# Performance work log

Hardware: AMD Instinct MI355X
Metric: run time of the kernel (lower is better)

Reference implementation:

```python
import jax, jax.numpy as jnp
import numpy as np
import math

B, N, T, F_IN, F_OUT = 32, 512, 12, 64, 64


def setup_inputs() -> dict:
    key = jax.random.key(0)
    k1, k2, k3 = jax.random.split(key, 3)
    x = jax.random.normal(k1, (B, N, T, F_IN), dtype=jnp.float32)
    adj = jax.random.uniform(k2, (N, N), dtype=jnp.float32)  # sym_norm_Adj_matrix
    W_theta = jax.random.normal(k3, (F_OUT, F_IN), dtype=jnp.float32) * (1.0 / math.sqrt(F_IN))
    return {"x": x, "adj": adj, "W_theta": W_theta}


def reference(x, adj, W_theta):
    # x: (B, N, T, F)
    b, n, t, f = x.shape
    scale = 1.0 / math.sqrt(f)
    # (B, T, N, F)
    xt = jnp.transpose(x, (0, 2, 1, 3))
    # attention scores per (batch, time): QK^T / sqrt(F), softmax over last dim,
    # then an extra 1/sqrt(F) scaling as in the original forward
    score = jnp.einsum('btnf,btmf->btnm', xt, xt) * scale
    att = jax.nn.softmax(score, axis=-1) * scale  # dropout p=0
    # post-softmax multiplicative adjacency mask, then aggregate neighbor features
    agg = jnp.einsum('btnm,btmf->btnf', adj[None, None] * att, xt)
    # Theta linear (no bias) + ReLU, back to (B, N, T, F_out)
    out = jax.nn.relu(jnp.einsum('btnf,of->btno', agg, W_theta))
    return jnp.transpose(out, (0, 2, 1, 3))
```

## Files before the change

### kernel.cpp

```cpp
#include <hip/hip_runtime.h>
#include <math.h>

#define NN 512
#define TT 12
#define FF 64

typedef float  f32x4   __attribute__((ext_vector_type(4)));
typedef float  f32x16  __attribute__((ext_vector_type(16)));
typedef short  short4v __attribute__((ext_vector_type(4)));
typedef short  short8v __attribute__((ext_vector_type(8)));
typedef _Float16 h16x4 __attribute__((ext_vector_type(4)));
typedef _Float16 h16x8 __attribute__((ext_vector_type(8)));
typedef unsigned int u32;
typedef u32    u32x4   __attribute__((ext_vector_type(4)));

static __device__ __forceinline__ u32 pkrtz(float a, float b) {
    u32 p;
    asm("v_cvt_pkrtz_f16_f32 %0, %1, %2" : "=v"(p) : "v"(a), "v"(b));
    return p;
}
static __device__ __forceinline__ void cvt4h(f32x4 v, short4v& h, short4v& lo) {
    h16x4 hh, ll;
    #pragma unroll
    for (int j = 0; j < 4; ++j) {
        _Float16 a = (_Float16)v[j];
        hh[j] = a;
        ll[j] = (_Float16)(v[j] - (float)a);
    }
    h  = __builtin_bit_cast(short4v, hh);
    lo = __builtin_bit_cast(short4v, ll);
}
static __device__ __forceinline__ short4v cvt4hi(f32x4 v) {
    h16x4 hh;
    #pragma unroll
    for (int j = 0; j < 4; ++j) hh[j] = (_Float16)v[j];
    return __builtin_bit_cast(short4v, hh);
}
static __device__ __forceinline__ short8v cat44(short4v a, short4v b) {
    return __builtin_shufflevector(a, b, 0, 1, 2, 3, 4, 5, 6, 7);
}
static __device__ __forceinline__ f32x16 mfmah(short8v a, short8v b, f32x16 c) {
    return __builtin_amdgcn_mfma_f32_32x32x16_f16(
        __builtin_bit_cast(h16x8, a), __builtin_bit_cast(h16x8, b), c, 0, 0, 0);
}

#define BUFSZ 17408
#define SMEM_BYTES 52736

__global__ __launch_bounds__(256, 3)
void sgcn19(const float* __restrict__ x, const float* __restrict__ adj,
            const float* __restrict__ W, float* __restrict__ out)
{
    __shared__ __align__(16) char smem[SMEM_BYTES];
    char* sA = smem;
    float* linvLDS = (float*)(smem + 3 * BUFSZ);

    const int d   = blockIdx.x;
    const int xcd = d & 7;
    const int s   = d >> 3;
    const int G   = xcd + 8 * (s >> 2);
    const int mem = s & 3;
    const int t = G % TT, b = G / TT;
    const int n0 = mem * 128;

    const int tid = threadIdx.x;
    const int w   = tid >> 6;
    const int l31 = tid & 31;
    const int hi2 = (tid >> 5) & 1;
    const int fq  = tid & 15;
    const int mq  = tid >> 4;
    const int myn = n0 + 32 * w + l31;

    const float K2 = 0.18033688011112042f;
    const float SH2 = 8.656170245333781f;

    const float* xnrow = x + ((size_t)(b * NN + myn) * TT + t) * FF;
    short8v xnH[4];
    #pragma unroll
    for (int ks = 0; ks < 4; ++ks) {
        f32x4 a0 = *(const f32x4*)(xnrow + ks * 16 + hi2 * 8);
        f32x4 a1 = *(const f32x4*)(xnrow + ks * 16 + hi2 * 8 + 4);
        xnH[ks] = cat44(cvt4hi(a0), cvt4hi(a1));
    }

    short4v sh[4];

#define STAGE_LOAD(M0, R0, R1, R2, R3)                                         \
    {                                                                          \
        const float* xs = x + ((size_t)(b * NN + (M0) + 4 * mq) * TT + t) * FF + 4 * fq; \
        R0 = *(const f32x4*)(xs);                                              \
        R1 = *(const f32x4*)(xs + TT * FF);                                    \
        R2 = *(const f32x4*)(xs + 2 * TT * FF);                                \
        R3 = *(const f32x4*)(xs + 3 * TT * FF);                                \
    }

#define STAGE_CONVERT(L0, L1, L2, L3)                                          \
    { sh[0] = cvt4hi(L0); sh[1] = cvt4hi(L1);                                  \
      sh[2] = cvt4hi(L2); sh[3] = cvt4hi(L3); }

#define STAGE_LDS_WRITE(DST)                                                   \
  {                                                                            \
    char* dKH = (DST);                                                         \
    char* dKT = (DST) + 8704;                                                  \
    _Pragma("unroll")                                                          \
    for (int j = 0; j < 4; ++j)                                                \
        *(short4v*)(dKH + ((4*mq+j)*68 + 4*fq) * 2) = sh[j];                   \
    _Pragma("unroll")                                                          \
    for (int j = 0; j < 4; ++j) {                                              \
        short4v th; th[0]=sh[0][j]; th[1]=sh[1][j]; th[2]=sh[2][j]; th[3]=sh[3][j]; \
        *(short4v*)(dKT + ((4*fq+j)*68 + 4*mq) * 2) = th;                      \
    }                                                                          \
  }

#define PROCESS_TILE(BASE, M0)                                                 \
  {                                                                            \
    const char* bKH = (BASE);                                                  \
    const char* bKT = (BASE) + 8704;                                           \
    const float* arow0 = adj + (size_t)myn * NN + (M0) + 4 * hi2;              \
    f32x4 a00 = *(const f32x4*)(arow0);                                        \
    f32x4 a01 = *(const f32x4*)(arow0 + 8);                                    \
    f32x4 a02 = *(const f32x4*)(arow0 + 16);                                   \
    f32x4 a03 = *(const f32x4*)(arow0 + 24);                                   \
    short8v pa[4];                                                             \
    f32x16 sc;                                                                 \
    _Pragma("unroll")                                                          \
    for (int i = 0; i < 16; ++i) sc[i] = 0.f;                                  \
    _Pragma("unroll")                                                          \
    for (int ks = 0; ks < 4; ++ks) {                                           \
        short4v k0 = *(const short4v*)(bKH + (l31 * 68 + ks*16 + hi2*8) * 2);  \
        short4v k1 = *(const short4v*)(bKH + (l31 * 68 + ks*16 + hi2*8 + 4) * 2); \
        sc = mfmah(cat44(k0, k1), xnH[ks], sc);                                \
    }                                                                          \
    const float* arow1 = adj + (size_t)myn * NN + (M0) + 32 + 4 * hi2;         \
    f32x4 a10 = *(const f32x4*)(arow1);                                        \
    f32x4 a11 = *(const f32x4*)(arow1 + 8);                                    \
    f32x4 a12 = *(const f32x4*)(arow1 + 16);                                   \
    f32x4 a13 = *(const f32x4*)(arow1 + 24);                                   \
    {                                                                          \
        float p[16];                                                           \
        _Pragma("unroll")                                                      \
        for (int r = 0; r < 16; ++r) {                                         \
            p[r] = __builtin_amdgcn_exp2f(sc[r] * K2 - SH2);                   \
            lp4[r & 3] += p[r];                                                \
        }                                                                      \
        p[0] *= a00[0]; p[1] *= a00[1]; p[2]  *= a00[2]; p[3]  *= a00[3];      \
        p[4] *= a01[0]; p[5] *= a01[1]; p[6]  *= a01[2]; p[7]  *= a01[3];      \
        p[8] *= a02[0]; p[9] *= a02[1]; p[10] *= a02[2]; p[11] *= a02[3];      \
        p[12]*= a03[0]; p[13]*= a03[1]; p[14] *= a03[2]; p[15] *= a03[3];      \
        u32x4 e, o;                                                            \
        e[0] = pkrtz(p[0],  p[1]);  e[1] = pkrtz(p[2],  p[3]);                 \
        e[2] = pkrtz(p[4],  p[5]);  e[3] = pkrtz(p[6],  p[7]);                 \
        o[0] = pkrtz(p[8],  p[9]);  o[1] = pkrtz(p[10], p[11]);                \
        o[2] = pkrtz(p[12], p[13]); o[3] = pkrtz(p[14], p[15]);                \
        pa[0] = __builtin_bit_cast(short8v, e);                                \
        pa[1] = __builtin_bit_cast(short8v, o);                                \
    }                                                                          \
    {                                                                          \
        short4v v0 = *(const short4v*)(bKT + (l31 * 68 + 4*hi2) * 2);          \
        short4v v1 = *(const short4v*)(bKT + (l31 * 68 + 8 + 4*hi2) * 2);      \
        agg0 = mfmah(pa[0], cat44(v0, v1), agg0);                              \
        short4v w0 = *(const short4v*)(bKT + ((32 + l31) * 68 + 4*hi2) * 2);   \
        short4v w1 = *(const short4v*)(bKT + ((32 + l31) * 68 + 8 + 4*hi2) * 2); \
        agg1 = mfmah(pa[0], cat44(w0, w1), agg1);                              \
        short4v v2 = *(const short4v*)(bKT + (l31 * 68 + 16 + 4*hi2) * 2);     \
        short4v v3 = *(const short4v*)(bKT + (l31 * 68 + 16 + 8 + 4*hi2) * 2); \
        agg0 = mfmah(pa[1], cat44(v2, v3), agg0);                              \
        short4v w2 = *(const short4v*)(bKT + ((32 + l31) * 68 + 16 + 4*hi2) * 2); \
        short4v w3 = *(const short4v*)(bKT + ((32 + l31) * 68 + 16 + 8 + 4*hi2) * 2); \
        agg1 = mfmah(pa[1], cat44(w2, w3), agg1);                              \
    }                                                                          \
    _Pragma("unroll")                                                          \
    for (int i = 0; i < 16; ++i) sc[i] = 0.f;                                  \
    _Pragma("unroll")                                                          \
    for (int ks = 0; ks < 4; ++ks) {                                           \
        short4v k0 = *(const short4v*)(bKH + ((32 + l31) * 68 + ks*16 + hi2*8) * 2); \
        short4v k1 = *(const short4v*)(bKH + ((32 + l31) * 68 + ks*16 + hi2*8 + 4) * 2); \
        sc = mfmah(cat44(k0, k1), xnH[ks], sc);                                \
    }                                                                          \
    {                                                                          \
        float p[16];                                                           \
        _Pragma("unroll")                                                      \
        for (int r = 0; r < 16; ++r) {                                         \
            p[r] = __builtin_amdgcn_exp2f(sc[r] * K2 - SH2);                   \
            lp4[r & 3] += p[r];                                                \
        }                                                                      \
        p[0] *= a10[0]; p[1] *= a10[1]; p[2]  *= a10[2]; p[3]  *= a10[3];      \
        p[4] *= a11[0]; p[5] *= a11[1]; p[6]  *= a11[2]; p[7]  *= a11[3];      \
        p[8] *= a12[0]; p[9] *= a12[1]; p[10] *= a12[2]; p[11] *= a12[3];      \
        p[12]*= a13[0]; p[13]*= a13[1]; p[14] *= a13[2]; p[15] *= a13[3];      \
        u32x4 e, o;                                                            \
        e[0] = pkrtz(p[0],  p[1]);  e[1] = pkrtz(p[2],  p[3]);                 \
        e[2] = pkrtz(p[4],  p[5]);  e[3] = pkrtz(p[6],  p[7]);                 \
        o[0] = pkrtz(p[8],  p[9]);  o[1] = pkrtz(p[10], p[11]);                \
        o[2] = pkrtz(p[12], p[13]); o[3] = pkrtz(p[14], p[15]);                \
        pa[2] = __builtin_bit_cast(short8v, e);                                \
        pa[3] = __builtin_bit_cast(short8v, o);                                \
    }                                                                          \
    {                                                                          \
        short4v v0 = *(const short4v*)(bKT + (l31 * 68 + 32 + 4*hi2) * 2);     \
        short4v v1 = *(const short4v*)(bKT + (l31 * 68 + 32 + 8 + 4*hi2) * 2); \
        agg0 = mfmah(pa[2], cat44(v0, v1), agg0);                              \
        short4v w0 = *(const short4v*)(bKT + ((32 + l31) * 68 + 32 + 4*hi2) * 2); \
        short4v w1 = *(const short4v*)(bKT + ((32 + l31) * 68 + 32 + 8 + 4*hi2) * 2); \
        agg1 = mfmah(pa[2], cat44(w0, w1), agg1);                              \
        short4v v2 = *(const short4v*)(bKT + (l31 * 68 + 48 + 4*hi2) * 2);     \
        short4v v3 = *(const short4v*)(bKT + (l31 * 68 + 48 + 8 + 4*hi2) * 2); \
        agg0 = mfmah(pa[3], cat44(v2, v3), agg0);                              \
        short4v w2 = *(const short4v*)(bKT + ((32 + l31) * 68 + 48 + 4*hi2) * 2); \
        short4v w3 = *(const short4v*)(bKT + ((32 + l31) * 68 + 48 + 8 + 4*hi2) * 2); \
        agg1 = mfmah(pa[3], cat44(w2, w3), agg1);                              \
    }                                                                          \
  }

    {
        f32x4 l0, l1, l2, l3;
        STAGE_LOAD(0, l0, l1, l2, l3)
        STAGE_CONVERT(l0, l1, l2, l3)
        STAGE_LDS_WRITE(smem)
        STAGE_LOAD(64, l0, l1, l2, l3)
        STAGE_CONVERT(l0, l1, l2, l3)
        STAGE_LDS_WRITE(smem + BUFSZ)
    }
    __syncthreads();

    float lp4[4] = {0.f, 0.f, 0.f, 0.f};
    f32x16 agg0, agg1;
    #pragma unroll
    for (int i = 0; i < 16; ++i) { agg0[i] = 0.f; agg1[i] = 0.f; }

    unsigned A = 0, B = BUFSZ, C = 2 * BUFSZ;
    for (int win = 0; win < 4; ++win) {
        const int ta = 2 * win;

        f32x4 q0, q1, q2, q3;
        if (win < 3) STAGE_LOAD((ta + 2) * 64, q0, q1, q2, q3)

        PROCESS_TILE(smem + A, ta * 64)

        f32x4 r0, r1, r2, r3;
        if (win < 3) {
            STAGE_CONVERT(q0, q1, q2, q3)
            STAGE_LDS_WRITE(smem + C)
            STAGE_LOAD((ta + 3) * 64, r0, r1, r2, r3)
        }

        PROCESS_TILE(smem + B, ta * 64 + 64)

        if (win < 3) STAGE_CONVERT(r0, r1, r2, r3)
        __syncthreads();
        if (win < 3) STAGE_LDS_WRITE(smem + A)
        __syncthreads();

        unsigned tmp = A; A = C; C = B; B = tmp;
    }

    float lpart = (lp4[0] + lp4[1]) + (lp4[2] + lp4[3]);
    float lf = lpart + __shfl_xor(lpart, 32);
    if (hi2 == 0) linvLDS[32 * w + l31] = 0.125f / lf;
    __syncthreads();

    #pragma unroll
    for (int r = 0; r < 16; ++r) {
        int row = 32 * w + (r & 3) + 8 * (r >> 2) + 4 * hi2;
        float nv = linvLDS[row];
        _Float16 h0 = (_Float16)(agg0[r] * nv);
        _Float16 h1 = (_Float16)(agg1[r] * nv);
        *(short*)(sA + (row * 68 + l31) * 2)      = __builtin_bit_cast(short, h0);
        *(short*)(sA + (row * 68 + 32 + l31) * 2) = __builtin_bit_cast(short, h1);
    }
    __syncthreads();

    short8v gH[4];
    #pragma unroll
    for (int ks = 0; ks < 4; ++ks) {
        short4v a0 = *(const short4v*)(sA + ((32*w + l31) * 68 + ks*16 + hi2*8) * 2);
        short4v a1 = *(const short4v*)(sA + ((32*w + l31) * 68 + ks*16 + hi2*8 + 4) * 2);
        gH[ks] = cat44(a0, a1);
    }

    #pragma unroll
    for (int ob = 0; ob < 2; ++ob) {
        short8v wHreg[4], wLreg[4];
        #pragma unroll
        for (int ks = 0; ks < 4; ++ks) {
            const float* wp = W + (size_t)(ob * 32 + l31) * FF + ks * 16 + hi2 * 8;
            f32x4 wa = *(const f32x4*)(wp);
            f32x4 wb = *(const f32x4*)(wp + 4);
            short4v h0, l0, h1, l1;
            cvt4h(wa, h0, l0);
            cvt4h(wb, h1, l1);
            wHreg[ks] = cat44(h0, h1);
            wLreg[ks] = cat44(l0, l1);
        }
        f32x16 oc;
        #pragma unroll
        for (int i = 0; i < 16; ++i) oc[i] = 0.f;
        #pragma unroll
        for (int ks = 0; ks < 4; ++ks) {
            oc = mfmah(gH[ks], wHreg[ks], oc);
            oc = mfmah(gH[ks], wLreg[ks], oc);
        }
        #pragma unroll
        for (int r = 0; r < 16; ++r) {
            int row = 32 * w + (r & 3) + 8 * (r >> 2) + 4 * hi2;
            out[((size_t)(b * NN + n0 + row) * TT + t) * FF + 32 * ob + l31] = fmaxf(oc[r], 0.f);
        }
    }
#undef STAGE_LOAD
#undef STAGE_CONVERT
#undef STAGE_LDS_WRITE
#undef PROCESS_TILE
}

extern "C" void kernel_launch(void* const* d_in, const int* in_sizes, int n_in,
                              void* d_out, int out_size, void* d_ws, size_t ws_size,
                              hipStream_t stream) {
    const float* x   = (const float*)d_in[0];
    const float* adj = (const float*)d_in[1];
    const float* W   = (const float*)d_in[2];
    float* outp = (float*)d_out;

    sgcn19<<<dim3(1536), dim3(256), 0, stream>>>(x, adj, W, outp);
}
```

Before: 77.44 us.

## Use 512-thread blocks covering 256 rows with double-buffered K tiles

Each block now has 512 threads (8 waves) and handles 256 query rows per (b,t) instead of 128, so every staged 64-row K/V tile in LDS is shared by twice as many rows and the grid is halved. The triple-buffered two-tiles-per-iteration pipeline becomes a simpler double buffer with one tile per iteration and a single barrier per tile. Each thread now loads two rows per stage instead of four, and the transposed LDS writes shrink to 2-element stores. This cuts redundant global loads of x and LDS traffic, at the cost of more threads per barrier, a shallower prefetch pipeline and possibly different occupancy.

```diff
diff --git a/kernel.cpp b/kernel.cpp
--- a/kernel.cpp
+++ b/kernel.cpp
@@ -7,6 +7,7 @@
 
 typedef float  f32x4   __attribute__((ext_vector_type(4)));
 typedef float  f32x16  __attribute__((ext_vector_type(16)));
+typedef short  short2v __attribute__((ext_vector_type(2)));
 typedef short  short4v __attribute__((ext_vector_type(4)));
 typedef short  short8v __attribute__((ext_vector_type(8)));
 typedef _Float16 h16x4 __attribute__((ext_vector_type(4)));
@@ -45,23 +46,23 @@
 }
 
 #define BUFSZ 17408
-#define SMEM_BYTES 52736
-
-__global__ __launch_bounds__(256, 3)
-void sgcn19(const float* __restrict__ x, const float* __restrict__ adj,
+#define SMEM_BYTES 35840
+
+__global__ __launch_bounds__(512, 4)
+void sgcn20(const float* __restrict__ x, const float* __restrict__ adj,
             const float* __restrict__ W, float* __restrict__ out)
 {
     __shared__ __align__(16) char smem[SMEM_BYTES];
     char* sA = smem;
-    float* linvLDS = (float*)(smem + 3 * BUFSZ);
+    float* linvLDS = (float*)(smem + 2 * BUFSZ);
 
     const int d   = blockIdx.x;
     const int xcd = d & 7;
     const int s   = d >> 3;
-    const int G   = xcd + 8 * (s >> 2);
-    const int mem = s & 3;
+    const int G   = xcd + 8 * (s >> 1);
+    const int mem = s & 1;
     const int t = G % TT, b = G / TT;
-    const int n0 = mem * 128;
+    const int n0 = mem * 256;
 
     const int tid = threadIdx.x;
     const int w   = tid >> 6;
@@ -83,32 +84,28 @@
         xnH[ks] = cat44(cvt4hi(a0), cvt4hi(a1));
     }
 
-    short4v sh[4];
-
-#define STAGE_LOAD(M0, R0, R1, R2, R3)                                         \
-    {                                                                          \
-        const float* xs = x + ((size_t)(b * NN + (M0) + 4 * mq) * TT + t) * FF + 4 * fq; \
+    short4v sh0, sh1;
+
+#define STAGE_LOAD(M0, R0, R1)                                                 \
+    {                                                                          \
+        const float* xs = x + ((size_t)(b * NN + (M0) + 2 * mq) * TT + t) * FF + 4 * fq; \
         R0 = *(const f32x4*)(xs);                                              \
         R1 = *(const f32x4*)(xs + TT * FF);                                    \
-        R2 = *(const f32x4*)(xs + 2 * TT * FF);                                \
-        R3 = *(const f32x4*)(xs + 3 * TT * FF);                                \
-    }
-
-#define STAGE_CONVERT(L0, L1, L2, L3)                                          \
-    { sh[0] = cvt4hi(L0); sh[1] = cvt4hi(L1);                                  \
-      sh[2] = cvt4hi(L2); sh[3] = cvt4hi(L3); }
+    }
+
+#define STAGE_CONVERT(L0, L1)                                                  \
+    { sh0 = cvt4hi(L0); sh1 = cvt4hi(L1); }
 
 #define STAGE_LDS_WRITE(DST)                                                   \
   {                                                                            \
     char* dKH = (DST);                                                         \
     char* dKT = (DST) + 8704;                                                  \
-    _Pragma("unroll")                                                          \
-    for (int j = 0; j < 4; ++j)                                                \
-        *(short4v*)(dKH + ((4*mq+j)*68 + 4*fq) * 2) = sh[j];                   \
+    *(short4v*)(dKH + ((2*mq+0)*68 + 4*fq) * 2) = sh0;                         \
+    *(short4v*)(dKH + ((2*mq+1)*68 + 4*fq) * 2) = sh1;                         \
     _Pragma("unroll")                                                          \
     for (int j = 0; j < 4; ++j) {                                              \
-        short4v th; th[0]=sh[0][j]; th[1]=sh[1][j]; th[2]=sh[2][j]; th[3]=sh[3][j]; \
-        *(short4v*)(dKT + ((4*fq+j)*68 + 4*mq) * 2) = th;                      \
+        short2v th; th[0] = sh0[j]; th[1] = sh1[j];                            \
+        *(short2v*)(dKT + ((4*fq+j)*68 + 2*mq) * 2) = th;                      \
     }                                                                          \
   }
 
@@ -213,13 +210,10 @@
   }
 
     {
-        f32x4 l0, l1, l2, l3;
-        STAGE_LOAD(0, l0, l1, l2, l3)
-        STAGE_CONVERT(l0, l1, l2, l3)
+        f32x4 l0, l1;
+        STAGE_LOAD(0, l0, l1)
+        STAGE_CONVERT(l0, l1)
         STAGE_LDS_WRITE(smem)
-        STAGE_LOAD(64, l0, l1, l2, l3)
-        STAGE_CONVERT(l0, l1, l2, l3)
-        STAGE_LDS_WRITE(smem + BUFSZ)
     }
     __syncthreads();
 
@@ -228,30 +222,19 @@
     #pragma unroll
     for (int i = 0; i < 16; ++i) { agg0[i] = 0.f; agg1[i] = 0.f; }
 
-    unsigned A = 0, B = BUFSZ, C = 2 * BUFSZ;
-    for (int win = 0; win < 4; ++win) {
-        const int ta = 2 * win;
-
-        f32x4 q0, q1, q2, q3;
-        if (win < 3) STAGE_LOAD((ta + 2) * 64, q0, q1, q2, q3)
-
-        PROCESS_TILE(smem + A, ta * 64)
-
-        f32x4 r0, r1, r2, r3;
-        if (win < 3) {
-            STAGE_CONVERT(q0, q1, q2, q3)
-            STAGE_LDS_WRITE(smem + C)
-            STAGE_LOAD((ta + 3) * 64, r0, r1, r2, r3)
+    unsigned bo = 0;
+    for (int mt = 0; mt < 8; ++mt) {
+        f32x4 p0, p1;
+        if (mt < 7) STAGE_LOAD((mt + 1) * 64, p0, p1)
+
+        PROCESS_TILE(smem + bo, mt * 64)
+
+        if (mt < 7) {
+            STAGE_CONVERT(p0, p1)
+            STAGE_LDS_WRITE(smem + (bo ^ BUFSZ))
         }
-
-        PROCESS_TILE(smem + B, ta * 64 + 64)
-
-        if (win < 3) STAGE_CONVERT(r0, r1, r2, r3)
         __syncthreads();
-        if (win < 3) STAGE_LDS_WRITE(smem + A)
-        __syncthreads();
-
-        unsigned tmp = A; A = C; C = B; B = tmp;
+        bo ^= BUFSZ;
     }
 
     float lpart = (lp4[0] + lp4[1]) + (lp4[2] + lp4[3]);
@@ -320,5 +303,5 @@
     const float* W   = (const float*)d_in[2];
     float* outp = (float*)d_out;
 
-    sgcn19<<<dim3(1536), dim3(256), 0, stream>>>(x, adj, W, outp);
-}
+    sgcn20<<<dim3(768), dim3(512), 0, stream>>>(x, adj, W, outp);
+}
```

Result: slower. 84.08 us (+8.6%).
